# Performance work log

Hardware: AMD Instinct MI355X
Metric: run time of the kernel (lower is better)

Reference implementation:

```python
import jax, jax.numpy as jnp
import numpy as np

N_NODES = 100000
N_EDGES = 1200000
N_DIM = 64


def setup_inputs() -> dict:
    key = jax.random.key(0)
    k1, k2, k3 = jax.random.split(key, 3)
    all_emb = jax.random.normal(k1, (N_NODES, N_DIM), dtype=jnp.float32) * 0.1
    edge_vals = jax.random.uniform(k2, (N_EDGES,), dtype=jnp.float32)
    edge_index = jax.random.randint(k3, (2, N_EDGES), 0, N_NODES, dtype=jnp.int64)
    return {"all_emb": all_emb, "edge_vals": edge_vals, "edge_index": edge_index, "n_layers": 3}


def _spmm(edge_vals, edge_index, x):
    # sparse.mm: out[dst] += val * x[src]; edge_index[0]=row(dst), edge_index[1]=col(src)
    dst, src = edge_index[0], edge_index[1]
    msgs = edge_vals[:, None] * x[src]          # [E, D] gather + scale
    return jax.ops.segment_sum(msgs, dst, num_segments=x.shape[0])


def reference(all_emb, edge_vals, edge_index, n_layers):
    # Fused layer-mean accumulation (avoids stacking all intermediates).
    emb = all_emb
    acc = all_emb
    for _ in range(n_layers):
        emb = _spmm(edge_vals, edge_index, emb)
        acc = acc + emb
    return acc / jnp.float32(n_layers + 1)
```

## Files before the change

### kernel.cpp

```cpp
#include <hip/hip_runtime.h>
#include <hip/hip_bf16.h>
#include <hip/hip_fp16.h>

#define D 64
#define P2_GRID 512
#define KITER 10
#define CHUNK (KITER*256)
#define KMAX 512
#define CAP 4096
#define SCAP 4608
#define CASTB 392

__device__ __forceinline__ unsigned f32_to_bf16_rne(float f) {
    unsigned u = __float_as_uint(f);
    return (u + 0x7FFFu + ((u >> 16) & 1u)) >> 16;
}
__device__ __forceinline__ float bflo(unsigned u) {
    return __uint_as_float(u << 16);
}
__device__ __forceinline__ float bfhi(unsigned u) {
    return __uint_as_float(u & 0xFFFF0000u);
}
__device__ __forceinline__ float hv(unsigned s) {
    return __half2float(__ushort_as_half((unsigned short)(s >> 17)));
}

__global__ __launch_bounds__(256) void p2_bin_cast(const int* __restrict__ ei,
                                                   const float* __restrict__ vals,
                                                   int* __restrict__ gcur,
                                                   unsigned long long* __restrict__ region,
                                                   const float4* __restrict__ emb4,
                                                   uint2* __restrict__ x0,
                                                   int n4, int E, int K) {
    __shared__ unsigned long long stage[CHUNK];
    __shared__ int hist[KMAX], sstart[KMAX], sbase[KMAX];
    __shared__ int wsum[4], woff[4];

    if (blockIdx.x >= P2_GRID) {
        int i0 = (blockIdx.x - P2_GRID) * 256 + threadIdx.x;
        for (int i = i0; i < n4; i += CASTB * 256) {
            float4 v = emb4[i];
            uint2 o;
            o.x = f32_to_bf16_rne(v.x) | (f32_to_bf16_rne(v.y) << 16);
            o.y = f32_to_bf16_rne(v.z) | (f32_to_bf16_rne(v.w) << 16);
            x0[i] = o;
        }
        return;
    }

    int t  = threadIdx.x;
    int c0 = blockIdx.x * CHUNK;
    int cnt = E - c0; if (cnt > CHUNK) cnt = CHUNK; if (cnt < 0) cnt = 0;

    hist[t] = 0; hist[t + 256] = 0;
    __syncthreads();

    unsigned long long ent[KITER];
    int rk[KITER];
    #pragma unroll
    for (int k = 0; k < KITER; ++k) {
        int i = t + k * 256;
        rk[k] = -1;
        if (i < cnt) {
            int e   = c0 + i;
            int dst = ei[e];
            int src = ei[E + e];
            unsigned h16 = (unsigned)__half_as_ushort(__float2half(vals[e]));
            int b = dst >> 8;
            ent[k] = ((unsigned long long)b << 41)
                   | ((unsigned long long)h16 << 25)
                   | ((unsigned long long)(dst & 0xFF) << 17)
                   | (unsigned long long)src;
            rk[k] = atomicAdd(&hist[b], 1);
        }
    }
    __syncthreads();

    int h0 = hist[2 * t], h1 = hist[2 * t + 1];
    int p  = h0 + h1;
    int lane = t & 63, w = t >> 6;
    int x = p;
    #pragma unroll
    for (int off = 1; off < 64; off <<= 1) {
        int y = __shfl_up(x, off, 64);
        if (lane >= off) x += y;
    }
    if (lane == 63) wsum[w] = x;
    __syncthreads();
    if (t < 4) {
        int e = 0;
        for (int i = 0; i < t; ++i) e += wsum[i];
        woff[t] = e;
    }
    __syncthreads();
    int excl = x - p + woff[w];
    sstart[2 * t]     = excl;
    sstart[2 * t + 1] = excl + h0;
    __syncthreads();

    for (int b = t; b < K; b += 256)
        sbase[b] = hist[b] ? atomicAdd(&gcur[b], hist[b]) : 0;

    #pragma unroll
    for (int k = 0; k < KITER; ++k) {
        if (rk[k] >= 0)
            stage[sstart[(int)(ent[k] >> 41)] + rk[k]] = ent[k];
    }
    __syncthreads();

    for (int i = t; i < cnt; i += 256) {
        unsigned long long e = stage[i];
        int b = (int)(e >> 41);
        int gidx = sbase[b] + (i - sstart[b]);
        if (gidx < CAP)
            region[((size_t)b << 12) | gidx] = e;
    }
}

__global__ __launch_bounds__(1024) void p3_csr(const unsigned long long* __restrict__ region,
                                               const int* __restrict__ gcur,
                                               unsigned* __restrict__ gslots,
                                               unsigned* __restrict__ rowinfo,
                                               int N) {
    __shared__ unsigned outstage[SCAP];
    __shared__ int rcnt[256], rstart[256];
    __shared__ int wsum[4], woff[4];
    __shared__ int stot;
    int b = blockIdx.x, t = threadIdx.x;
    int cnt = gcur[b]; if (cnt > CAP) cnt = CAP;
    const unsigned long long* reg = region + ((size_t)b << 12);

    if (t < 256) rcnt[t] = 0;
    __syncthreads();

    unsigned long long ent[4];
    int rk[4];
    #pragma unroll
    for (int k = 0; k < 4; ++k) {
        int i = t + k * 1024;
        rk[k] = -1;
        if (i < cnt) {
            ent[k] = reg[i];
            rk[k]  = atomicAdd(&rcnt[(int)(ent[k] >> 17) & 0xFF], 1);
        }
    }
    __syncthreads();

    int rc = 0, rcp = 0, x = 0, rs = 0;
    int lane = t & 63, w = t >> 6;
    if (t < 256) {
        rc  = rcnt[t]; if (rc > 56) rc = 56;
        rcp = (rc + 7) & ~7;
        x = rcp;
        #pragma unroll
        for (int off = 1; off < 64; off <<= 1) {
            int y = __shfl_up(x, off, 64);
            if (lane >= off) x += y;
        }
        if (lane == 63) wsum[w] = x;
    }
    __syncthreads();
    if (t < 4) {
        int e = 0;
        for (int i = 0; i < t; ++i) e += wsum[i];
        woff[t] = e;
    }
    __syncthreads();
    if (t < 256) {
        rs = x - rcp + woff[w];
        rstart[t] = rs;
        if (t == 255) stot = rs + rcp;
    }
    __syncthreads();

    #pragma unroll
    for (int k = 0; k < 4; ++k) {
        if (rk[k] >= 0 && rk[k] < 56) {
            int pos = rstart[(int)(ent[k] >> 17) & 0xFF] + rk[k];
            if (pos < SCAP)
                outstage[pos] = ((unsigned)((ent[k] >> 25) & 0x7FFF) << 17)
                              | (unsigned)(ent[k] & 0x1FFFF);
        }
    }
    if (t < 256) {
        for (int i = rs + rc; i < rs + rcp; ++i)
            if (i >= 0 && i < SCAP) outstage[i] = 0u;
    }
    __syncthreads();

    int ptot = stot; if (ptot > SCAP) ptot = SCAP;
    size_t gb = (size_t)b * SCAP;
    for (int i = t; i < ptot; i += 1024)
        gslots[gb + i] = outstage[i];
    if (t < 256) {
        int row = (b << 8) | t;
        if (row < N) {
            int ni = rcp >> 3;
            if (rs >= SCAP) ni = 0;
            else if (rs + (ni << 3) > SCAP) ni = (SCAP - rs) >> 3;
            rowinfo[row] = ((unsigned)(gb + (size_t)rs) << 4) | (unsigned)ni;
        }
    }
}

__global__ __launch_bounds__(256) void spmm4e(const uint2* __restrict__ xs2,
                                              const unsigned* __restrict__ gslots,
                                              const unsigned* __restrict__ rowinfo,
                                              uint2* __restrict__ nexts2,
                                              const uint2* __restrict__ x0s2,
                                              const uint2* __restrict__ h1s2,
                                              float4* __restrict__ outf4,
                                              int mode, int N) {
    int gid = blockIdx.x * blockDim.x + threadIdx.x;
    int row = __builtin_amdgcn_readfirstlane(gid >> 6);
    if (row >= N) return;
    int lane = gid & 63;
    int q = lane >> 4;
    int p = lane & 15;
    unsigned info = rowinfo[row];
    int niter = (int)(info & 15u);
    const unsigned* s = gslots + (info >> 4);

    float a0 = 0.f, a1 = 0.f, a2 = 0.f, a3 = 0.f;
    for (int it = 0; it < niter; ++it, s += 8) {
        unsigned s0 = s[0], s1 = s[1], s2 = s[2], s3 = s[3],
                 s4 = s[4], s5 = s[5], s6 = s[6], s7 = s[7];
        unsigned wa = (q & 2) ? ((q & 1) ? s3 : s2) : ((q & 1) ? s1 : s0);
        unsigned wb = (q & 2) ? ((q & 1) ? s7 : s6) : ((q & 1) ? s5 : s4);
        uint2 ga = xs2[((size_t)(wa & 0x1FFFFu) << 4) | p];
        uint2 gb = xs2[((size_t)(wb & 0x1FFFFu) << 4) | p];
        float va = hv(wa), vb = hv(wb);
        a0 += va * bflo(ga.x); a1 += va * bfhi(ga.x);
        a2 += va * bflo(ga.y); a3 += va * bfhi(ga.y);
        a0 += vb * bflo(gb.x); a1 += vb * bfhi(gb.x);
        a2 += vb * bflo(gb.y); a3 += vb * bfhi(gb.y);
    }

    a0 += __shfl_xor(a0, 16, 64); a1 += __shfl_xor(a1, 16, 64);
    a2 += __shfl_xor(a2, 16, 64); a3 += __shfl_xor(a3, 16, 64);
    a0 += __shfl_xor(a0, 32, 64); a1 += __shfl_xor(a1, 32, 64);
    a2 += __shfl_xor(a2, 32, 64); a3 += __shfl_xor(a3, 32, 64);

    if (lane < 16) {
        int o = (row << 4) | p;
        if (mode != 2) {
            uint2 r;
            r.x = f32_to_bf16_rne(a0) | (f32_to_bf16_rne(a1) << 16);
            r.y = f32_to_bf16_rne(a2) | (f32_to_bf16_rne(a3) << 16);
            nexts2[o] = r;
        } else {
            uint2 x0 = x0s2[o], h1 = h1s2[o], x2 = xs2[o];
            float4 r;
            r.x = (bflo(x0.x) + bflo(h1.x) + bflo(x2.x) + a0) * 0.25f;
            r.y = (bfhi(x0.x) + bfhi(h1.x) + bfhi(x2.x) + a1) * 0.25f;
            r.z = (bflo(x0.y) + bflo(h1.y) + bflo(x2.y) + a2) * 0.25f;
            r.w = (bfhi(x0.y) + bfhi(h1.y) + bfhi(x2.y) + a3) * 0.25f;
            outf4[o] = r;
        }
    }
}

extern "C" void kernel_launch(void* const* d_in, const int* in_sizes, int n_in,
                              void* d_out, int out_size, void* d_ws, size_t ws_size,
                              hipStream_t stream) {
    const float* all_emb   = (const float*)d_in[0];
    const float* edge_vals = (const float*)d_in[1];
    const int*   edge_idx  = (const int*)d_in[2];

    const int E = in_sizes[1];
    const int n = out_size;
    const int N = n / D;
    const int K = (N + 255) >> 8;
    float* out = (float*)d_out;

    unsigned long long* region = (unsigned long long*)d_ws;
    unsigned* gslots  = (unsigned*)(region + (size_t)K * CAP);
    unsigned* rowinfo = gslots + (size_t)K * SCAP;
    int*      gcur    = (int*)(rowinfo + N);
    unsigned* X0      = (unsigned*)(gcur + ((K + 1) & ~1));
    unsigned* X1      = X0 + n / 2;
    unsigned* X2      = X1 + n / 2;

    const int TB = 256;
    const int grid_spmm = (N * 64 + TB - 1) / TB;

    hipMemsetAsync(gcur, 0, (size_t)K * sizeof(int), stream);
    p2_bin_cast<<<P2_GRID + CASTB, TB, 0, stream>>>(edge_idx, edge_vals, gcur, region,
                                                    (const float4*)all_emb, (uint2*)X0,
                                                    n / 4, E, K);
    p3_csr<<<K, 1024, 0, stream>>>(region, gcur, gslots, rowinfo, N);

    spmm4e<<<grid_spmm, TB, 0, stream>>>((const uint2*)X0, gslots, rowinfo,
                                         (uint2*)X1, nullptr, nullptr, nullptr, 0, N);
    spmm4e<<<grid_spmm, TB, 0, stream>>>((const uint2*)X1, gslots, rowinfo,
                                         (uint2*)X2, nullptr, nullptr, nullptr, 1, N);
    spmm4e<<<grid_spmm, TB, 0, stream>>>((const uint2*)X2, gslots, rowinfo,
                                         nullptr, (const uint2*)X0,
                                         (const uint2*)X1, (float4*)out, 2, N);
}
```

Measured before the change: 233.5 us.

## Split bf16 embeddings into four column slices for cache-local SpMM gathers

```diff
diff --git a/kernel.cpp b/kernel.cpp
--- a/kernel.cpp
+++ b/kernel.cpp
@@ -3,6 +3,7 @@
 #include <hip/hip_fp16.h>
 
 #define D 64
+#define NSL 4
 #define P2_GRID 512
 #define KITER 10
 #define CHUNK (KITER*256)
@@ -15,6 +16,9 @@
     unsigned u = __float_as_uint(f);
     return (u + 0x7FFFu + ((u >> 16) & 1u)) >> 16;
 }
+__device__ __forceinline__ unsigned pk(float a, float b) {
+    return f32_to_bf16_rne(a) | (f32_to_bf16_rne(b) << 16);
+}
 __device__ __forceinline__ float bflo(unsigned u) {
     return __uint_as_float(u << 16);
 }
@@ -30,20 +34,27 @@
                                                    int* __restrict__ gcur,
                                                    unsigned long long* __restrict__ region,
                                                    const float4* __restrict__ emb4,
-                                                   uint2* __restrict__ x0,
-                                                   int n4, int E, int K) {
+                                                   uint4* __restrict__ x0q,
+                                                   int N, int E, int K) {
     __shared__ unsigned long long stage[CHUNK];
     __shared__ int hist[KMAX], sstart[KMAX], sbase[KMAX];
     __shared__ int wsum[4], woff[4];
 
     if (blockIdx.x >= P2_GRID) {
-        int i0 = (blockIdx.x - P2_GRID) * 256 + threadIdx.x;
-        for (int i = i0; i < n4; i += CASTB * 256) {
-            float4 v = emb4[i];
-            uint2 o;
-            o.x = f32_to_bf16_rne(v.x) | (f32_to_bf16_rne(v.y) << 16);
-            o.y = f32_to_bf16_rne(v.z) | (f32_to_bf16_rne(v.w) << 16);
-            x0[i] = o;
+        int j0 = (blockIdx.x - P2_GRID) * 256 + threadIdx.x;
+        int total = N * 4;
+        for (int j = j0; j < total; j += CASTB * 256) {
+            int node = j >> 2, s = j & 3;
+            const float4* sp = emb4 + (size_t)node * 16 + s * 4;
+            float4 v0 = sp[0], v1 = sp[1], v2 = sp[2], v3 = sp[3];
+            uint4 o0, o1;
+            o0.x = pk(v0.x, v0.y); o0.y = pk(v0.z, v0.w);
+            o0.z = pk(v1.x, v1.y); o0.w = pk(v1.z, v1.w);
+            o1.x = pk(v2.x, v2.y); o1.y = pk(v2.z, v2.w);
+            o1.z = pk(v3.x, v3.y); o1.w = pk(v3.z, v3.w);
+            size_t base = ((size_t)s * N + node) * 2;
+            x0q[base]     = o0;
+            x0q[base + 1] = o1;
         }
         return;
     }
@@ -203,59 +214,50 @@
     }
 }
 
-__global__ __launch_bounds__(256) void spmm4e(const uint2* __restrict__ xs2,
-                                              const unsigned* __restrict__ gslots,
-                                              const unsigned* __restrict__ rowinfo,
-                                              uint2* __restrict__ nexts2,
-                                              const uint2* __restrict__ x0s2,
-                                              const uint2* __restrict__ h1s2,
-                                              float4* __restrict__ outf4,
-                                              int mode, int N) {
-    int gid = blockIdx.x * blockDim.x + threadIdx.x;
-    int row = __builtin_amdgcn_readfirstlane(gid >> 6);
+__global__ __launch_bounds__(1024) void spmm_slice(const unsigned* __restrict__ xs,
+                                                   const unsigned* __restrict__ gslots,
+                                                   const unsigned* __restrict__ rowinfo,
+                                                   unsigned* __restrict__ nexts,
+                                                   const unsigned* __restrict__ x0s,
+                                                   const unsigned* __restrict__ h1s,
+                                                   float* __restrict__ outf,
+                                                   int mode, int N) {
+    int g = blockIdx.x;
+    int slice = (g & 7) >> 1;
+    int rg = ((g >> 3) << 1) | (g & 1);
+    int w = __builtin_amdgcn_readfirstlane((int)threadIdx.x >> 6);
+    int row = rg * 16 + w;
     if (row >= N) return;
-    int lane = gid & 63;
-    int q = lane >> 4;
-    int p = lane & 15;
+    int lane = threadIdx.x & 63;
+    int e = lane >> 3, dp = lane & 7;
+
     unsigned info = rowinfo[row];
     int niter = (int)(info & 15u);
     const unsigned* s = gslots + (info >> 4);
-
-    float a0 = 0.f, a1 = 0.f, a2 = 0.f, a3 = 0.f;
+    const unsigned* xb = xs + (size_t)slice * N * 8 + dp;
+
+    float a0 = 0.f, a1 = 0.f;
     for (int it = 0; it < niter; ++it, s += 8) {
-        unsigned s0 = s[0], s1 = s[1], s2 = s[2], s3 = s[3],
-                 s4 = s[4], s5 = s[5], s6 = s[6], s7 = s[7];
-        unsigned wa = (q & 2) ? ((q & 1) ? s3 : s2) : ((q & 1) ? s1 : s0);
-        unsigned wb = (q & 2) ? ((q & 1) ? s7 : s6) : ((q & 1) ? s5 : s4);
-        uint2 ga = xs2[((size_t)(wa & 0x1FFFFu) << 4) | p];
-        uint2 gb = xs2[((size_t)(wb & 0x1FFFFu) << 4) | p];
-        float va = hv(wa), vb = hv(wb);
-        a0 += va * bflo(ga.x); a1 += va * bfhi(ga.x);
-        a2 += va * bflo(ga.y); a3 += va * bfhi(ga.y);
-        a0 += vb * bflo(gb.x); a1 += vb * bfhi(gb.x);
-        a2 += vb * bflo(gb.y); a3 += vb * bfhi(gb.y);
-    }
-
+        unsigned sl = s[e];
+        unsigned x  = xb[(size_t)(sl & 0x1FFFFu) << 3];
+        float v = hv(sl);
+        a0 = fmaf(v, bflo(x), a0);
+        a1 = fmaf(v, bfhi(x), a1);
+    }
+    a0 += __shfl_xor(a0, 8, 64);  a1 += __shfl_xor(a1, 8, 64);
     a0 += __shfl_xor(a0, 16, 64); a1 += __shfl_xor(a1, 16, 64);
-    a2 += __shfl_xor(a2, 16, 64); a3 += __shfl_xor(a3, 16, 64);
     a0 += __shfl_xor(a0, 32, 64); a1 += __shfl_xor(a1, 32, 64);
-    a2 += __shfl_xor(a2, 32, 64); a3 += __shfl_xor(a3, 32, 64);
-
-    if (lane < 16) {
-        int o = (row << 4) | p;
+
+    if (e == 0) {
+        size_t o = ((size_t)slice * N + row) * 8 + dp;
         if (mode != 2) {
-            uint2 r;
-            r.x = f32_to_bf16_rne(a0) | (f32_to_bf16_rne(a1) << 16);
-            r.y = f32_to_bf16_rne(a2) | (f32_to_bf16_rne(a3) << 16);
-            nexts2[o] = r;
+            nexts[o] = pk(a0, a1);
         } else {
-            uint2 x0 = x0s2[o], h1 = h1s2[o], x2 = xs2[o];
-            float4 r;
-            r.x = (bflo(x0.x) + bflo(h1.x) + bflo(x2.x) + a0) * 0.25f;
-            r.y = (bfhi(x0.x) + bfhi(h1.x) + bfhi(x2.x) + a1) * 0.25f;
-            r.z = (bflo(x0.y) + bflo(h1.y) + bflo(x2.y) + a2) * 0.25f;
-            r.w = (bfhi(x0.y) + bfhi(h1.y) + bfhi(x2.y) + a3) * 0.25f;
-            outf4[o] = r;
+            unsigned ux0 = x0s[o], uh1 = h1s[o], ux2 = xs[o];
+            float r0 = (bflo(ux0) + bflo(uh1) + bflo(ux2) + a0) * 0.25f;
+            float r1 = (bfhi(ux0) + bfhi(uh1) + bfhi(ux2) + a1) * 0.25f;
+            float2 r; r.x = r0; r.y = r1;
+            *(float2*)&outf[((size_t)row << 6) | (slice << 4) | (dp << 1)] = r;
         }
     }
 }
@@ -281,20 +283,19 @@
     unsigned* X1      = X0 + n / 2;
     unsigned* X2      = X1 + n / 2;
 
-    const int TB = 256;
-    const int grid_spmm = (N * 64 + TB - 1) / TB;
+    const int nrg = (N + 15) / 16;
+    const int grid_sl = 8 * ((nrg + 1) / 2);
 
     hipMemsetAsync(gcur, 0, (size_t)K * sizeof(int), stream);
-    p2_bin_cast<<<P2_GRID + CASTB, TB, 0, stream>>>(edge_idx, edge_vals, gcur, region,
-                                                    (const float4*)all_emb, (uint2*)X0,
-                                                    n / 4, E, K);
+    p2_bin_cast<<<P2_GRID + CASTB, 256, 0, stream>>>(edge_idx, edge_vals, gcur, region,
+                                                     (const float4*)all_emb, (uint4*)X0,
+                                                     N, E, K);
     p3_csr<<<K, 1024, 0, stream>>>(region, gcur, gslots, rowinfo, N);
 
-    spmm4e<<<grid_spmm, TB, 0, stream>>>((const uint2*)X0, gslots, rowinfo,
-                                         (uint2*)X1, nullptr, nullptr, nullptr, 0, N);
-    spmm4e<<<grid_spmm, TB, 0, stream>>>((const uint2*)X1, gslots, rowinfo,
-                                         (uint2*)X2, nullptr, nullptr, nullptr, 1, N);
-    spmm4e<<<grid_spmm, TB, 0, stream>>>((const uint2*)X2, gslots, rowinfo,
-                                         nullptr, (const uint2*)X0,
-                                         (const uint2*)X1, (float4*)out, 2, N);
-}
+    spmm_slice<<<grid_sl, 1024, 0, stream>>>(X0, gslots, rowinfo,
+                                             X1, nullptr, nullptr, nullptr, 0, N);
+    spmm_slice<<<grid_sl, 1024, 0, stream>>>(X1, gslots, rowinfo,
+                                             X2, nullptr, nullptr, nullptr, 1, N);
+    spmm_slice<<<grid_sl, 1024, 0, stream>>>(X2, gslots, rowinfo,
+                                             nullptr, X0, X1, out, 2, N);
+}
```

New measurement: 425.9 us. 1.82x slower.
